# Kernel tuning notes

Hardware: AMD Instinct MI355X
Metric: run time of the kernel (lower is better)

The kernel has to match this reference:

```python
import jax, jax.numpy as jnp
import numpy as np

K = 2  # k-MIS hops (matches init k)


def _khop_min(mr, row, col, n, k):
    # k rounds of: min over in-neighbors (scatter_min row->col), then min with self
    for _ in range(k):
        neigh = jax.ops.segment_min(mr[row], col, num_segments=n)
        mr = jnp.minimum(mr, neigh)
    return mr


def _score_and_rank(x, lin_w, lin_b, row, col, n, k):
    score = jax.nn.sigmoid(x @ lin_w + lin_b)  # [n,1] linear scorer
    s = score[:, 0]
    # 'greedy' heuristic: s' = s / ((A+I)^k 1)
    ks = jnp.ones_like(s)
    for _ in range(k):
        ks = ks + jax.ops.segment_sum(ks[row], col, num_segments=n)
    upd = s / ks
    perm = jnp.argsort(-upd)  # descending: higher score -> lower rank
    rank = jnp.zeros(n, jnp.int32).at[perm].set(jnp.arange(n, dtype=jnp.int32))
    return score, rank


def _kmis_cluster(row, col, rank, n, k):
    nI = jnp.int32(n)

    def cond(state):
        return ~jnp.all(state[1])

    def body(state):
        mis, mask, mr = state
        mr = _khop_min(mr, row, col, n, k)
        mis = mis | (rank == mr)
        m = mis.astype(jnp.int32)
        for _ in range(k):  # propagate coverage k hops (scatter_max)
            neigh = jax.ops.segment_max(m[row], col, num_segments=n)
            m = jnp.maximum(m, jnp.clip(neigh, 0, 1))
        mask = m > 0
        mr = jnp.where(mask, nI, rank)
        return mis, mask, mr

    mis0 = jnp.zeros(n, bool)
    mis, _, _ = jax.lax.while_loop(cond, body, (mis0, mis0, rank))
    # clustering: propagate min rank of MIS nodes k hops
    mr = _khop_min(jnp.where(mis, rank, nI), row, col, n, k)
    mis_idx = jnp.nonzero(mis)[0]  # eager (data-dependent size, like torch)
    rank_mis = rank[mis_idx]
    order = jnp.argsort(rank_mis)
    # unique(min_rank).inverse then perm[clusters] == index into MIS nodes (node order)
    cluster = order[jnp.searchsorted(rank_mis[order], mr)]
    return mis_idx, cluster


def setup_inputs() -> dict:
    key = jax.random.key(0)
    k1, k2, k3, _ = jax.random.split(key, 4)
    n, e, d = 100000, 1600000, 256
    x = jax.random.normal(k1, (n, d), jnp.float32)
    edge_index = jax.random.randint(k2, (2, e), 0, n, jnp.int32)
    lin_w = jax.random.normal(k3, (d, 1), jnp.float32) * 0.05
    lin_b = jnp.zeros((1,), jnp.float32)
    return {"x": x, "edge_index": edge_index, "lin_w": lin_w, "lin_b": lin_b}


def reference(x, edge_index, lin_w, lin_b):
    n = x.shape[0]
    row, col = edge_index[0], edge_index[1]
    score, rank = _score_and_rank(x, lin_w, lin_b, row, col, n, K)
    mis_idx, cluster = _kmis_cluster(row, col, rank, n, K)
    # pool edges: relabel endpoints, coalesce duplicates with 'sum', drop self-loops
    pairs = jnp.stack([cluster[row], cluster[col]], axis=1)
    uniq, inv = jnp.unique(pairs, axis=0, return_inverse=True)
    val = jax.ops.segment_sum(jnp.ones(row.shape[0], jnp.float32), inv.reshape(-1), num_segments=uniq.shape[0])
    keep = uniq[:, 0] != uniq[:, 1]
    new_edge_index = uniq[keep].T
    new_edge_attr = val[keep]
    # pool nodes: score_passthrough='before', aggr_x=None -> select MIS rows
    x_pool = (x * score)[mis_idx]
    return x_pool, new_edge_index, new_edge_attr
```

## Files before the change

kernel.cpp:

```cpp
#include <hip/hip_runtime.h>
#include <math.h>

#define BLOCK 256
#define EGRID 2048
#define SG    512
#define NTHE (EGRID*BLOCK)
#define NWVE (NTHE/64)
#define INF_ 0x7fffffff
#define TB   6000
#define AWMAX 224
#define DENSE_ITERS 6

struct KParams {
  const float* x;
  const int*   ei;
  const float* w;
  const float* bb;
  float* out;
  int n, e, d, out_size;
  int* ws;
  long long ws_ints;
};

struct Lay {
  float* score; int *ks1,*cursor;
  int *keyA,*idxA,*keyB,*idxB,*lrank;
  int *rank,*mr,*t1,*mis,*mm,*misPre,*r2c,*clus,*colPtr,*rowPtr;
  unsigned *bh,*dtot,*dbase,*btot,*bbase;
  int *cnts,*colSrc,*rowDst,*pairCnt;
  long long unionBase;
};

__device__ __host__ inline Lay mklay(int* ws, int n, int e) {
  Lay L;
  L.score=(float*)ws;
  L.ks1   = ws + (size_t)1*n;
  L.cursor= ws + (size_t)2*n;
  L.keyA  = ws + (size_t)3*n;
  L.idxA  = ws + (size_t)4*n;
  L.keyB  = ws + (size_t)5*n;
  L.idxB  = ws + (size_t)6*n;
  L.lrank = ws + (size_t)7*n;
  L.rank  = ws + (size_t)8*n;
  L.mr    = ws + (size_t)9*n;
  L.t1    = ws + (size_t)10*n;
  L.mis   = ws + (size_t)11*n;
  L.mm    = ws + (size_t)12*n;
  L.misPre= ws + (size_t)13*n;
  L.r2c   = ws + (size_t)14*n;
  L.clus  = ws + (size_t)15*n;
  L.colPtr= ws + (size_t)16*n;
  L.rowPtr= ws + (size_t)17*n + 64;
  int* sm = ws + (size_t)18*n + 128;
  L.bh    = (unsigned*)sm;
  L.dtot  = L.bh + 256*SG;
  L.dbase = L.dtot + 256;
  L.btot  = L.dbase + 256;
  L.bbase = L.btot + SG;
  L.cnts  = (int*)(L.bbase + SG);
  L.unionBase = 18ll*n + 128 + 256ll*SG + 512 + 2ll*SG + 16;
  L.colSrc  = ws + L.unionBase;
  L.rowDst  = L.colSrc + e;
  L.pairCnt = ws + L.unionBase;
  return L;
}

__device__ inline int gmin_(const int* __restrict__ s, const int* __restrict__ val,
                            int p, int pe, int m) {
  for (; p+3 < pe; p += 4) {
    int a0=s[p],a1=s[p+1],a2=s[p+2],a3=s[p+3];
    int t0=val[a0],t1=val[a1],t2=val[a2],t3=val[a3];
    t0=min(t0,t1); t2=min(t2,t3); t0=min(t0,t2); if (t0<m) m=t0;
  }
  for (; p<pe; ++p){ int t=val[s[p]]; if (t<m) m=t; }
  return m;
}
__device__ inline int gor_(const int* __restrict__ s, const int* __restrict__ val,
                           int p, int pe, int m) {
  for (; p+3 < pe; p += 4) m |= val[s[p]] | val[s[p+1]] | val[s[p+2]] | val[s[p+3]];
  for (; p<pe; ++p) m |= val[s[p]];
  return m;
}
__device__ inline int gsum_(const int* __restrict__ s, const int* __restrict__ val,
                            int p, int pe, int m) {
  for (; p+3 < pe; p += 4) m += val[s[p]] + val[s[p+1]] + val[s[p+2]] + val[s[p+3]];
  for (; p<pe; ++p) m += val[s[p]];
  return m;
}

__device__ inline int btotPrefix(const unsigned* btot, int upto) {
  __shared__ int red[256];
  int tid = threadIdx.x;
  int partial = 0;
  for (int idx = tid; idx < upto; idx += 256) partial += (int)btot[idx];
  __syncthreads();
  red[tid] = partial; __syncthreads();
  for (int off = 128; off > 0; off >>= 1) { if (tid < off) red[tid] += red[tid+off]; __syncthreads(); }
  int r = red[0]; __syncthreads();
  return r;
}

__global__ __launch_bounds__(BLOCK) void k_score(KParams P) {
  Lay L = mklay(P.ws, P.n, P.e);
  int gid = blockIdx.x*BLOCK + threadIdx.x;
  int lane = gid & 63, gwv = gid >> 6;
  int d4 = P.d >> 2;
  double bconst = (double)P.bb[0];
  const float4* w4 = (const float4*)P.w;
  for (int v = gwv; v < P.n; v += NWVE) {
    const float4* xr = (const float4*)(P.x + (size_t)v*P.d);
    double s = 0.0;
    for (int q = lane; q < d4; q += 64) {
      float4 xv = xr[q], wv = w4[q];
      s += (double)xv.x*wv.x + (double)xv.y*wv.y + (double)xv.z*wv.z + (double)xv.w*wv.w;
    }
    for (int off = 32; off > 0; off >>= 1) s += __shfl_down(s, off);
    if (lane == 0) L.score[v] = (float)(1.0/(1.0+exp(-(s+bconst))));
  }
  for (int v = gid; v < P.n; v += NTHE) L.ks1[v] = 0;
}

__global__ __launch_bounds__(BLOCK) void k_degree(KParams P) {
  Lay L = mklay(P.ws, P.n, P.e);
  const int* col = P.ei + P.e;
  int gid = blockIdx.x*BLOCK + threadIdx.x;
  for (int j = gid; j < P.e; j += NTHE) atomicAdd(&L.ks1[col[j]], 1);
}

__global__ __launch_bounds__(BLOCK) void k_scan1(KParams P) {
  Lay L = mklay(P.ws, P.n, P.e);
  __shared__ int lds[256];
  int tid = threadIdx.x, bid = blockIdx.x;
  int chunk = (P.n + SG - 1)/SG;
  int ig = bid*chunk + tid;
  bool valid = (tid < chunk) && (ig < P.n);
  int v2 = valid ? L.ks1[ig] : 0;
  lds[tid] = v2; __syncthreads();
  for (int off = 1; off < 256; off <<= 1) {
    int t = (tid >= off) ? lds[tid-off] : 0; __syncthreads();
    lds[tid] += t; __syncthreads();
  }
  if (valid) L.colPtr[ig] = lds[tid] - v2;
  if (tid == 0) L.btot[bid] = (unsigned)lds[255];
}

__global__ __launch_bounds__(BLOCK) void k_scan3(KParams P) {
  Lay L = mklay(P.ws, P.n, P.e);
  int tid = threadIdx.x, bid = blockIdx.x;
  int base = btotPrefix(L.btot, bid);
  int chunk = (P.n + SG - 1)/SG;
  int ig = bid*chunk + tid;
  if (tid < chunk && ig < P.n) {
    int cp = L.colPtr[ig] + base;
    L.colPtr[ig] = cp; L.cursor[ig] = cp; L.ks1[ig] += 1;
  }
  if (bid == 0 && tid == 0) L.colPtr[P.n] = P.e;
}

__global__ __launch_bounds__(BLOCK) void k_csr(KParams P) {
  Lay L = mklay(P.ws, P.n, P.e);
  const int* row = P.ei; const int* col = P.ei + P.e;
  int gid = blockIdx.x*BLOCK + threadIdx.x;
  for (int j = gid; j < P.e; j += NTHE) {
    int pos = atomicAdd(&L.cursor[col[j]], 1);
    L.colSrc[pos] = row[j];
  }
}

__global__ __launch_bounds__(BLOCK) void k_keygen(KParams P) {
  Lay L = mklay(P.ws, P.n, P.e);
  int v = blockIdx.x*BLOCK + threadIdx.x;
  if (v >= P.n) return;
  int s = gsum_(L.colSrc, L.ks1, L.colPtr[v], L.colPtr[v+1], L.ks1[v]);
  float upd = L.score[v] / (float)s;
  unsigned u = __float_as_uint(upd);
  u = (u & 0x80000000u) ? (~u) : (u | 0x80000000u);
  ((unsigned*)L.keyA)[v] = ~u;
  ((unsigned*)L.idxA)[v] = (unsigned)v;
}

__global__ __launch_bounds__(BLOCK) void k_sort_local(KParams P, int pass) {
  Lay L = mklay(P.ws, P.n, P.e);
  __shared__ int ldsH[1024];
  int tid = threadIdx.x, bid = blockIdx.x, lane = tid & 63, wib = tid >> 6;
  unsigned* sk = (pass & 1) ? (unsigned*)L.keyB : (unsigned*)L.keyA;
  int shift = pass*8;
  for (int i = tid; i < 1024; i += BLOCK) ldsH[i] = 0;
  __syncthreads();
  int chunk = (P.n + SG - 1)/SG;
  int ig = bid*chunk + tid;
  bool valid = (tid < chunk) && (ig < P.n);
  int dig = 0;
  if (valid) dig = (int)((sk[ig] >> shift) & 255u);
  unsigned long long mmask = __ballot(valid);
  for (int b = 0; b < 8; ++b) {
    unsigned long long bm = __ballot((dig >> b) & 1);
    mmask &= ((dig >> b) & 1) ? bm : ~bm;
  }
  int lp = 0;
  if (valid) {
    lp = __popcll(mmask & ((1ull << lane) - 1ull));
    if (lp == 0) ldsH[wib*256 + dig] = __popcll(mmask);
  }
  __syncthreads();
  if (tid < 256) {
    int c0=ldsH[tid], c1=ldsH[256+tid], c2=ldsH[512+tid], c3=ldsH[768+tid];
    ldsH[tid]=0; ldsH[256+tid]=c0; ldsH[512+tid]=c0+c1; ldsH[768+tid]=c0+c1+c2;
    L.bh[(size_t)tid*SG + bid] = (unsigned)(c0+c1+c2+c3);
  }
  __syncthreads();
  if (valid) ((unsigned*)L.lrank)[ig] = (unsigned)(ldsH[wib*256 + dig] + lp);
}

__global__ __launch_bounds__(BLOCK) void k_sort_scan1(KParams P) {
  Lay L = mklay(P.ws, P.n, P.e);
  int g = blockIdx.x*BLOCK + threadIdx.x;
  int dg = g >> 6, lane = g & 63;
  if (dg >= 256) return;
  unsigned running = 0;
  for (int r = 0; r < SG/64; ++r) {
    unsigned v = L.bh[(size_t)dg*SG + r*64 + lane];
    unsigned incl = v;
    for (int off = 1; off < 64; off <<= 1) { unsigned t = __shfl_up(incl, off); if (lane >= off) incl += t; }
    L.bh[(size_t)dg*SG + r*64 + lane] = incl - v + running;
    running += __shfl(incl, 63);
  }
  if (lane == 0) L.dtot[dg] = running;
}

__global__ __launch_bounds__(BLOCK) void k_sort_scatter(KParams P, int pass) {
  Lay L = mklay(P.ws, P.n, P.e);
  __shared__ unsigned sdb[256];
  unsigned *sk,*si,*dk,*di;
  if (pass & 1) { sk=(unsigned*)L.keyB; si=(unsigned*)L.idxB; dk=(unsigned*)L.keyA; di=(unsigned*)L.idxA; }
  else          { sk=(unsigned*)L.keyA; si=(unsigned*)L.idxA; dk=(unsigned*)L.keyB; di=(unsigned*)L.idxB; }
  int tid = threadIdx.x, bid = blockIdx.x;
  unsigned myv = L.dtot[tid];
  sdb[tid] = myv; __syncthreads();
  for (int off = 1; off < 256; off <<= 1) {
    unsigned t = (tid >= off) ? sdb[tid-off] : 0u; __syncthreads();
    sdb[tid] += t; __syncthreads();
  }
  unsigned excl = sdb[tid] - myv; __syncthreads();
  sdb[tid] = excl; __syncthreads();
  int chunk = (P.n + SG - 1)/SG;
  int ig = bid*chunk + tid;
  if (tid < chunk && ig < P.n) {
    unsigned key = sk[ig];
    int dig = (int)((key >> (pass*8)) & 255u);
    unsigned pos = sdb[dig] + L.bh[(size_t)dig*SG + bid] + ((unsigned*)L.lrank)[ig];
    dk[pos] = key; di[pos] = si[ig];
  }
}

__global__ __launch_bounds__(BLOCK) void k_rankinit(KParams P) {
  Lay L = mklay(P.ws, P.n, P.e);
  int i = blockIdx.x*BLOCK + threadIdx.x;
  if (blockIdx.x == 0 && threadIdx.x == 0) {
    L.cnts[4] = P.n;
    L.cnts[5] = 0;
  }
  if (i >= P.n) return;
  int v = (int)((unsigned*)L.idxA)[i];
  L.rank[v] = i;
  L.mm[v] = i;
  L.mis[v] = 0;
}

__global__ __launch_bounds__(BLOCK) void k_dmin(KParams P, int t) {
  Lay L = mklay(P.ws, P.n, P.e);
  if (L.cnts[4+(t&1)] <= TB) return;
  int w = blockIdx.x*BLOCK + threadIdx.x;
  if (w >= P.n) return;
  L.mr[w] = gmin_(L.colSrc, L.mm, L.colPtr[w], L.colPtr[w+1], L.mm[w]);
}
__global__ __launch_bounds__(BLOCK) void k_dsel(KParams P, int t) {
  Lay L = mklay(P.ws, P.n, P.e);
  int q = t & 1;
  int A = L.cnts[4+q];
  if (A <= TB) return;
  int i = blockIdx.x*BLOCK + threadIdx.x;
  if (i >= A) return;
  int v = (t == 0) ? i : (q ? L.keyB : L.keyA)[i];
  int m2 = gmin_(L.colSrc, L.mr, L.colPtr[v], L.colPtr[v+1], L.mr[v]);
  if (L.rank[v] == m2) L.mis[v] = 1;
}
__global__ __launch_bounds__(BLOCK) void k_dor(KParams P, int t) {
  Lay L = mklay(P.ws, P.n, P.e);
  int q = t & 1;
  if (L.cnts[4+q] <= TB) return;
  int w = blockIdx.x*BLOCK + threadIdx.x;
  if (blockIdx.x == 0 && threadIdx.x == 0) L.cnts[4+(1-q)] = 0;
  if (w >= P.n) return;
  L.t1[w] = gor_(L.colSrc, L.mis, L.colPtr[w], L.colPtr[w+1], L.mis[w]);
}
__global__ __launch_bounds__(BLOCK) void k_drb(KParams P, int t) {
  Lay L = mklay(P.ws, P.n, P.e);
  int q = t & 1;
  int A = L.cnts[4+q];
  int* act  = (t == 0) ? (int*)0 : (q ? L.keyB : L.keyA);
  int* nact = q ? L.keyA : L.keyB;
  int gid = blockIdx.x*BLOCK + threadIdx.x;
  if (A <= TB) {
    for (int i = gid; i < A; i += (P.n + BLOCK - 1)/BLOCK*BLOCK) nact[i] = act[i];
    if (gid == 0) L.cnts[4+(1-q)] = A;
    return;
  }
  int lane = threadIdx.x & 63;
  bool aliveF = false; int v = 0;
  if (gid < A) {
    v = (t == 0) ? gid : act[gid];
    int dead = gor_(L.colSrc, L.t1, L.colPtr[v], L.colPtr[v+1], L.t1[v]);
    if (dead) L.mm[v] = INF_; else aliveF = true;
  }
  unsigned long long mk = __ballot(aliveF);
  int cntw = __popcll(mk);
  if (cntw) {
    int fl = __ffsll((unsigned long long)mk) - 1;
    int base = 0;
    if (lane == fl) base = atomicAdd(&L.cnts[4+(1-q)], cntw);
    base = __shfl(base, fl);
    if (aliveF) nact[base + __popcll(mk & ((1ull<<lane)-1ull))] = v;
  }
}

__global__ __launch_bounds__(BLOCK) void k_tcomp1(KParams P) {
  Lay L = mklay(P.ws, P.n, P.e);
  __shared__ int lds[256];
  int tid = threadIdx.x, bid = blockIdx.x;
  int chunk = (P.n + SG - 1)/SG;
  int ig = bid*chunk + tid;
  bool valid = (tid < chunk) && (ig < P.n);
  int f = 0;
  if (valid) { int v = (int)((unsigned*)L.idxA)[ig]; f = (L.mm[v] != INF_) ? 1 : 0; }
  lds[tid] = f; __syncthreads();
  for (int off = 1; off < 256; off <<= 1) {
    int t = (tid >= off) ? lds[tid-off] : 0; __syncthreads();
    lds[tid] += t; __syncthreads();
  }
  if (valid) L.t1[ig] = lds[tid] - f;
  if (tid == 0) L.btot[bid] = (unsigned)lds[255];
}
__global__ __launch_bounds__(BLOCK) void k_tcomp3(KParams P) {
  Lay L = mklay(P.ws, P.n, P.e);
  int tid = threadIdx.x, bid = blockIdx.x;
  int base = btotPrefix(L.btot, bid);
  int chunk = (P.n + SG - 1)/SG;
  int ig = bid*chunk + tid;
  if (tid < chunk && ig < P.n) {
    int v = (int)((unsigned*)L.idxA)[ig];
    if (L.mm[v] != INF_) {
      int pos = L.t1[ig] + base;
      L.lrank[pos] = v;
      L.cursor[v] = pos;
    } else L.cursor[v] = -1;
  }
  int A = L.cnts[4];
  if (A > 0) {
    int AW = (A + 31) >> 5;
    int AWP = (AW + 3) & ~3;
    unsigned* bs = (unsigned*)L.rowDst;
    long long tot = (long long)A * AWP;
    for (long long idx = (long long)bid*BLOCK + tid; idx < tot; idx += (long long)SG*BLOCK) bs[idx] = 0u;
  }
}
__global__ __launch_bounds__(BLOCK) void k_tbuild(KParams P) {
  Lay L = mklay(P.ws, P.n, P.e);
  int A = L.cnts[4];
  if (A <= 0) return;
  int AW = (A + 31) >> 5;
  int AWP = (AW + 3) & ~3;
  unsigned* bs = (unsigned*)L.rowDst;
  const int* __restrict__ cp = L.colPtr;
  const int* __restrict__ cs = L.colSrc;
  const int* __restrict__ nodeIdx = L.cursor;
  int gid = blockIdx.x*BLOCK + threadIdx.x;
  int lane = gid & 63, gwv = gid >> 6;
  int nW = (gridDim.x*BLOCK) >> 6;
  for (int i = gwv; i < A; i += nW) {
    int v = L.lrank[i];
    unsigned* row = bs + (size_t)i*AWP;
    if (lane == 0) atomicOr(&row[i >> 5], 1u << (i & 31));
    int p0 = cp[v], p1 = cp[v+1];
    for (int p = p0 + lane; p < p1; p += 64) {
      int u = cs[p];
      int j = nodeIdx[u];
      if (j >= 0) atomicOr(&row[j >> 5], 1u << (j & 31));
      int p3 = cp[u+1];
      for (int p2 = cp[u]; p2 < p3; ++p2) {
        int w2 = cs[p2];
        int j2 = nodeIdx[w2];
        if (j2 >= 0) atomicOr(&row[j2 >> 5], 1u << (j2 & 31));
      }
    }
  }
}
__global__ __launch_bounds__(1024) void k_trounds(KParams P) {
  Lay L = mklay(P.ws, P.n, P.e);
  __shared__ __align__(16) unsigned aliveW[AWMAX];
  __shared__ __align__(16) unsigned selW[AWMAX];
  __shared__ int scnt;
  int A = L.cnts[4];
  if (A <= 0) return;
  int AW = (A + 31) >> 5;
  int AWP = (AW + 3) & ~3;
  const unsigned* __restrict__ bs = (const unsigned*)L.rowDst;
  const int* __restrict__ S = L.lrank;
  const uint4* __restrict__ a4 = (const uint4*)aliveW;
  const uint4* __restrict__ s4 = (const uint4*)selW;
  int tid = threadIdx.x;
  for (int w = tid; w < AWP; w += 1024) {
    int base = w*32; int c = A - base;
    aliveW[w] = (c >= 32) ? 0xffffffffu : ((c > 0) ? ((1u << c) - 1u) : 0u);
  }
  __syncthreads();
  int ng = AWP >> 2;
  for (int rounds = 0; rounds < 8192; ++rounds) {
    for (int w = tid; w < AWP; w += 1024) selW[w] = 0u;
    if (tid == 0) scnt = 0;
    __syncthreads();
    for (int i = tid; i < A; i += 1024) {
      if ((aliveW[i>>5] >> (i&31)) & 1u) {
        const unsigned* __restrict__ row = bs + (size_t)i*AWP;
        const uint4* __restrict__ r4 = (const uint4*)row;
        int wl = i >> 5;
        int nf = wl >> 2;
        unsigned any = 0;
        int g = 0;
        for (; g + 2 <= nf; g += 2) {
          uint4 a = r4[g],   b = r4[g+1];
          uint4 av = a4[g],  bv = a4[g+1];
          unsigned r0 = (a.x&av.x)|(a.y&av.y)|(a.z&av.z)|(a.w&av.w);
          unsigned r1 = (b.x&bv.x)|(b.y&bv.y)|(b.z&bv.z)|(b.w&bv.w);
          any = r0 | r1;
          if (any) break;
        }
        if (!any && g < nf) {
          uint4 a = r4[g]; uint4 av = a4[g];
          any = (a.x&av.x)|(a.y&av.y)|(a.z&av.z)|(a.w&av.w);
        }
        if (!any) {
          for (int w2 = nf << 2; w2 < wl; ++w2) any |= row[w2] & aliveW[w2];
          if (!any && (i & 31)) any = row[wl] & aliveW[wl] & ((1u << (i&31)) - 1u);
        }
        if (!any) { atomicOr(&selW[i>>5], 1u << (i&31)); L.mis[S[i]] = 1; }
      }
    }
    __syncthreads();
    int surv = 0;
    for (int i = tid; i < A; i += 1024) {
      if ((aliveW[i>>5] >> (i&31)) & 1u) {
        const uint4* __restrict__ r4 = (const uint4*)(bs + (size_t)i*AWP);
        unsigned dead = 0;
        int g = 0;
        for (; g + 2 <= ng; g += 2) {
          uint4 a = r4[g],  b = r4[g+1];
          uint4 sa = s4[g], sb = s4[g+1];
          dead |= (a.x&sa.x)|(a.y&sa.y)|(a.z&sa.z)|(a.w&sa.w)
                | (b.x&sb.x)|(b.y&sb.y)|(b.z&sb.z)|(b.w&sb.w);
        }
        if (g < ng) {
          uint4 a = r4[g]; uint4 sa = s4[g];
          dead |= (a.x&sa.x)|(a.y&sa.y)|(a.z&sa.z)|(a.w&sa.w);
        }
        if (dead) atomicAnd(&aliveW[i>>5], ~(1u << (i&31)));
        else ++surv;
      }
    }
    if (surv) atomicAdd(&scnt, surv);
    __syncthreads();
    int sc = scnt;
    __syncthreads();
    if (sc == 0) break;
  }
}

__global__ __launch_bounds__(BLOCK) void k_scanM1(KParams P) {
  Lay L = mklay(P.ws, P.n, P.e);
  __shared__ int lds[256];
  int tid = threadIdx.x, bid = blockIdx.x;
  int chunk = (P.n + SG - 1)/SG;
  int ig = bid*chunk + tid;
  bool valid = (tid < chunk) && (ig < P.n);
  int v2 = 0;
  if (valid) {
    v2 = L.mis[ig];
    L.mm[ig] = v2 ? L.rank[ig] : P.n;
  }
  lds[tid] = v2; __syncthreads();
  for (int off = 1; off < 256; off <<= 1) {
    int t = (tid >= off) ? lds[tid-off] : 0; __syncthreads();
    lds[tid] += t; __syncthreads();
  }
  if (valid) L.misPre[ig] = lds[tid] - v2;
  if (tid == 0) L.btot[bid] = (unsigned)lds[255];
}
__global__ __launch_bounds__(BLOCK) void k_fin1(KParams P) {
  Lay L = mklay(P.ws, P.n, P.e);
  int v = blockIdx.x*BLOCK + threadIdx.x;
  if (v >= P.n) return;
  L.t1[v] = gmin_(L.colSrc, L.mm, L.colPtr[v], L.colPtr[v+1], L.mm[v]);
}
__global__ __launch_bounds__(BLOCK) void k_fin2(KParams P) {
  Lay L = mklay(P.ws, P.n, P.e);
  int v = blockIdx.x*BLOCK + threadIdx.x;
  if (v >= P.n) return;
  L.mr[v] = gmin_(L.colSrc, L.t1, L.colPtr[v], L.colPtr[v+1], L.t1[v]);
}
__global__ __launch_bounds__(BLOCK) void k_scanM3(KParams P) {
  Lay L = mklay(P.ws, P.n, P.e);
  int tid = threadIdx.x, bid = blockIdx.x;
  int base = btotPrefix(L.btot, bid);
  int total = btotPrefix(L.btot, SG);
  int chunk = (P.n + SG - 1)/SG;
  int ig = bid*chunk + tid;
  if (tid < chunk && ig < P.n) {
    int p = L.misPre[ig] + base;
    L.misPre[ig] = p;
    if (L.mis[ig]) L.r2c[L.rank[ig]] = p;
  }
  if (bid == 0 && tid == 0) L.cnts[2] = total;
}

__global__ __launch_bounds__(BLOCK) void k_clus(KParams P) {
  Lay L = mklay(P.ws, P.n, P.e);
  int gid = blockIdx.x*BLOCK + threadIdx.x;
  int M = L.cnts[2];
  long long M2 = (long long)M*M;
  for (int v = gid; v < P.n; v += NTHE) {
    int r3 = L.mr[v];
    L.clus[v] = (r3 >= 0 && r3 < P.n) ? L.r2c[r3] : 0;
  }
  bool pairOk = (M > 0) && (M2 < 0x7fffffffll) && (L.unionBase + M2 <= P.ws_ints);
  if (pairOk) {
    int m2i = (int)M2;
    for (int i = gid; i < m2i; i += NTHE) L.pairCnt[i] = 0;
  }
}

__global__ __launch_bounds__(BLOCK) void k_pair(KParams P) {
  Lay L = mklay(P.ws, P.n, P.e);
  int M = L.cnts[2];
  long long M2 = (long long)M*M;
  bool pairOk = (M > 0) && (M2 < 0x7fffffffll) && (L.unionBase + M2 <= P.ws_ints);
  if (!pairOk) return;
  const int* row = P.ei; const int* col = P.ei + P.e;
  int gid = blockIdx.x*BLOCK + threadIdx.x;
  for (int j = gid; j < P.e; j += NTHE) {
    int a = L.clus[row[j]], b2 = L.clus[col[j]];
    atomicAdd(&L.pairCnt[a*M + b2], 1);
  }
}

__global__ __launch_bounds__(BLOCK) void k_keep1(KParams P) {
  Lay L = mklay(P.ws, P.n, P.e);
  __shared__ int lds[256];
  int tid = threadIdx.x, bid = blockIdx.x;
  int M = L.cnts[2];
  long long M2 = (long long)M*M;
  bool pairOk = (M > 0) && (M2 < 0x7fffffffll) && (L.unionBase + M2 <= P.ws_ints);
  int m2i = pairOk ? (int)M2 : 0;
  int chunkP = pairOk ? (m2i + SG - 1)/SG : 0;
  int pstart = bid*chunkP; if (pstart > m2i) pstart = m2i;
  int pend = pstart + chunkP; if (pend > m2i) pend = m2i;
  int localKeep = 0;
  for (int i = pstart + tid; i < pend; i += BLOCK) {
    int c = L.pairCnt[i];
    if (c > 0 && (i / M) != (i % M)) ++localKeep;
  }
  lds[tid] = localKeep; __syncthreads();
  for (int off = 128; off > 0; off >>= 1) { if (tid < off) lds[tid] += lds[tid+off]; __syncthreads(); }
  if (tid == 0) L.btot[bid] = (unsigned)lds[0];
}

__global__ __launch_bounds__(BLOCK) void k_edges(KParams P) {
  Lay L = mklay(P.ws, P.n, P.e);
  __shared__ int lds[256];
  int tid = threadIdx.x, bid = blockIdx.x;
  int M = L.cnts[2];
  long long M2 = (long long)M*M;
  bool pairOk = (M > 0) && (M2 < 0x7fffffffll) && (L.unionBase + M2 <= P.ws_ints);
  if (!pairOk) return;
  int base = btotPrefix(L.btot, bid);
  int EK = btotPrefix(L.btot, SG);
  int m2i = (int)M2;
  int chunkP = (m2i + SG - 1)/SG;
  int pstart = bid*chunkP; if (pstart > m2i) pstart = m2i;
  int pend = pstart + chunkP; if (pend > m2i) pend = m2i;
  size_t eBase = (size_t)M * (size_t)P.d;
  bool outOk = (eBase + 3ull*(size_t)EK <= (size_t)P.out_size);
  int running2 = base;
  for (int t0 = pstart; t0 < pend; t0 += BLOCK) {
    int i = t0 + tid;
    int c = 0, kept = 0, a = 0, b2 = 0;
    if (i < pend) {
      c = L.pairCnt[i];
      a = i / M; b2 = i % M;
      kept = (c > 0 && a != b2) ? 1 : 0;
    }
    lds[tid] = kept; __syncthreads();
    for (int off = 1; off < 256; off <<= 1) {
      int t = (tid >= off) ? lds[tid-off] : 0; __syncthreads();
      lds[tid] += t; __syncthreads();
    }
    int incl = lds[tid], tot = lds[255];
    if (kept && outOk) {
      int j2 = running2 + incl - 1;
      P.out[eBase + (size_t)j2] = (float)a;
      P.out[eBase + (size_t)EK + (size_t)j2] = (float)b2;
      P.out[eBase + 2ull*(size_t)EK + (size_t)j2] = (float)c;
    }
    running2 += tot;
    __syncthreads();
  }
}

__global__ __launch_bounds__(BLOCK) void k_xpool(KParams P) {
  Lay L = mklay(P.ws, P.n, P.e);
  int gid = blockIdx.x*BLOCK + threadIdx.x;
  int lane = gid & 63, gwv = gid >> 6;
  int M = L.cnts[2];
  int d4 = P.d >> 2;
  size_t eBase = (size_t)M * (size_t)P.d;
  if (eBase > (size_t)P.out_size) return;
  for (int v = gwv; v < P.n; v += NWVE) {
    if (L.mis[v]) {
      int p = L.misPre[v];
      float sc = L.score[v];
      const float4* xr = (const float4*)(P.x + (size_t)v*P.d);
      float4* outr = (float4*)P.out + (size_t)p*d4;
      for (int q = lane; q < d4; q += 64) {
        float4 xv = xr[q];
        outr[q] = make_float4(xv.x*sc, xv.y*sc, xv.z*sc, xv.w*sc);
      }
    }
  }
}

extern "C" void kernel_launch(void* const* d_in, const int* in_sizes, int n_in,
                              void* d_out, int out_size, void* d_ws, size_t ws_size,
                              hipStream_t stream) {
  KParams P;
  P.x  = (const float*)d_in[0];
  P.ei = (const int*)d_in[1];
  P.w  = (const float*)d_in[2];
  P.bb = (const float*)d_in[3];
  P.out = (float*)d_out;
  P.d = in_sizes[2];
  P.n = in_sizes[0] / P.d;
  P.e = in_sizes[1] / 2;
  P.out_size = out_size;
  P.ws = (int*)d_ws;
  P.ws_ints = (long long)(ws_size / 4);
  const int nblk = (P.n + BLOCK - 1) / BLOCK;

  k_score <<<EGRID, BLOCK, 0, stream>>>(P);
  k_degree<<<EGRID, BLOCK, 0, stream>>>(P);
  k_scan1 <<<SG,    BLOCK, 0, stream>>>(P);
  k_scan3 <<<SG,    BLOCK, 0, stream>>>(P);
  k_csr   <<<EGRID, BLOCK, 0, stream>>>(P);
  k_keygen<<<nblk,  BLOCK, 0, stream>>>(P);
  for (int pass = 0; pass < 4; ++pass) {
    k_sort_local  <<<SG, BLOCK, 0, stream>>>(P, pass);
    k_sort_scan1  <<<64, BLOCK, 0, stream>>>(P);
    k_sort_scatter<<<SG, BLOCK, 0, stream>>>(P, pass);
  }
  k_rankinit<<<nblk, BLOCK, 0, stream>>>(P);
  for (int t = 0; t < DENSE_ITERS; ++t) {
    k_dmin <<<nblk, BLOCK, 0, stream>>>(P, t);
    k_dsel <<<nblk, BLOCK, 0, stream>>>(P, t);
    k_dor  <<<nblk, BLOCK, 0, stream>>>(P, t);
    k_drb  <<<nblk, BLOCK, 0, stream>>>(P, t);
  }
  k_tcomp1 <<<SG,   BLOCK, 0, stream>>>(P);
  k_tcomp3 <<<SG,   BLOCK, 0, stream>>>(P);
  k_tbuild <<<nblk, BLOCK, 0, stream>>>(P);
  k_trounds<<<1,    1024,  0, stream>>>(P);
  k_scanM1<<<SG, BLOCK, 0, stream>>>(P);
  k_fin1  <<<nblk, BLOCK, 0, stream>>>(P);
  k_fin2  <<<nblk, BLOCK, 0, stream>>>(P);
  k_scanM3<<<SG, BLOCK, 0, stream>>>(P);
  k_clus <<<EGRID, BLOCK, 0, stream>>>(P);
  k_pair <<<EGRID, BLOCK, 0, stream>>>(P);
  k_keep1<<<SG,    BLOCK, 0, stream>>>(P);
  k_edges<<<SG,    BLOCK, 0, stream>>>(P);
  k_xpool<<<EGRID, BLOCK, 0, stream>>>(P);
}
```

Before: 968.9 us.

## Build transposed conflict bitmatrix and kill nodes via selected-row OR in tail rounds

During the dense tail MIS phase, the build kernel now also fills a transposed bit matrix, when workspace allows, by issuing mirrored atomicOr operations. Each round records the selected nodes in a shared list. Dead nodes are then found by OR-ing the transposed rows of only those nodes into a shared deadW mask, instead of every alive node scanning its full row against the selection mask. A per-node resume pointer (pw) also lets the lower-rank check skip words already known to be clear. In exchange, the build does twice the atomics and writes a second matrix, the check loop drops its uint4 vectorization, and the resume pointer is stored as an unsigned char.

Measured after the change: 1.023 ms. 5.5% more time.

```diff
diff --git a/kernel.cpp b/kernel.cpp
--- a/kernel.cpp
+++ b/kernel.cpp
@@ -9,6 +9,7 @@
 #define INF_ 0x7fffffff
 #define TB   6000
 #define AWMAX 224
+#define TBCAP 7168
 #define DENSE_ITERS 6
 
 struct KParams {
@@ -362,6 +363,11 @@
     unsigned* bs = (unsigned*)L.rowDst;
     long long tot = (long long)A * AWP;
     for (long long idx = (long long)bid*BLOCK + tid; idx < tot; idx += (long long)SG*BLOCK) bs[idx] = 0u;
+    bool transOk = (L.unionBase + 2ll*P.e + tot <= P.ws_ints);
+    if (transOk) {
+      unsigned* tr = (unsigned*)(P.ws + L.unionBase + 2ll*P.e);
+      for (long long idx = (long long)bid*BLOCK + tid; idx < tot; idx += (long long)SG*BLOCK) tr[idx] = 0u;
+    }
   }
 }
 __global__ __launch_bounds__(BLOCK) void k_tbuild(KParams P) {
@@ -371,6 +377,8 @@
   int AW = (A + 31) >> 5;
   int AWP = (AW + 3) & ~3;
   unsigned* bs = (unsigned*)L.rowDst;
+  bool transOk = (L.unionBase + 2ll*P.e + (long long)A*AWP <= P.ws_ints);
+  unsigned* tr = transOk ? (unsigned*)(P.ws + L.unionBase + 2ll*P.e) : (unsigned*)0;
   const int* __restrict__ cp = L.colPtr;
   const int* __restrict__ cs = L.colSrc;
   const int* __restrict__ nodeIdx = L.cursor;
@@ -380,17 +388,28 @@
   for (int i = gwv; i < A; i += nW) {
     int v = L.lrank[i];
     unsigned* row = bs + (size_t)i*AWP;
-    if (lane == 0) atomicOr(&row[i >> 5], 1u << (i & 31));
+    unsigned ibit = 1u << (i & 31);
+    int iw = i >> 5;
+    if (lane == 0) {
+      atomicOr(&row[iw], ibit);
+      if (tr) atomicOr(&tr[(size_t)i*AWP + iw], ibit);
+    }
     int p0 = cp[v], p1 = cp[v+1];
     for (int p = p0 + lane; p < p1; p += 64) {
       int u = cs[p];
       int j = nodeIdx[u];
-      if (j >= 0) atomicOr(&row[j >> 5], 1u << (j & 31));
+      if (j >= 0) {
+        atomicOr(&row[j >> 5], 1u << (j & 31));
+        if (tr) atomicOr(&tr[(size_t)j*AWP + iw], ibit);
+      }
       int p3 = cp[u+1];
       for (int p2 = cp[u]; p2 < p3; ++p2) {
         int w2 = cs[p2];
         int j2 = nodeIdx[w2];
-        if (j2 >= 0) atomicOr(&row[j2 >> 5], 1u << (j2 & 31));
+        if (j2 >= 0) {
+          atomicOr(&row[j2 >> 5], 1u << (j2 & 31));
+          if (tr) atomicOr(&tr[(size_t)j2*AWP + iw], ibit);
+        }
       }
     }
   }
@@ -399,72 +418,81 @@
   Lay L = mklay(P.ws, P.n, P.e);
   __shared__ __align__(16) unsigned aliveW[AWMAX];
   __shared__ __align__(16) unsigned selW[AWMAX];
-  __shared__ int scnt;
+  __shared__ __align__(16) unsigned deadW[AWMAX];
+  __shared__ int selList[TBCAP];
+  __shared__ unsigned char pw[TBCAP];
+  __shared__ int scnt, selCnt;
   int A = L.cnts[4];
   if (A <= 0) return;
   int AW = (A + 31) >> 5;
   int AWP = (AW + 3) & ~3;
   const unsigned* __restrict__ bs = (const unsigned*)L.rowDst;
+  bool transOk = (L.unionBase + 2ll*P.e + (long long)A*AWP <= P.ws_ints);
+  const unsigned* __restrict__ tr = (const unsigned*)(P.ws + L.unionBase + 2ll*P.e);
   const int* __restrict__ S = L.lrank;
-  const uint4* __restrict__ a4 = (const uint4*)aliveW;
-  const uint4* __restrict__ s4 = (const uint4*)selW;
   int tid = threadIdx.x;
   for (int w = tid; w < AWP; w += 1024) {
     int base = w*32; int c = A - base;
     aliveW[w] = (c >= 32) ? 0xffffffffu : ((c > 0) ? ((1u << c) - 1u) : 0u);
   }
+  for (int i = tid; i < A; i += 1024) pw[i] = 0;
   __syncthreads();
-  int ng = AWP >> 2;
   for (int rounds = 0; rounds < 8192; ++rounds) {
-    for (int w = tid; w < AWP; w += 1024) selW[w] = 0u;
-    if (tid == 0) scnt = 0;
+    for (int w = tid; w < AWP; w += 1024) { selW[w] = 0u; deadW[w] = 0u; }
+    if (tid == 0) { scnt = 0; selCnt = 0; }
     __syncthreads();
     for (int i = tid; i < A; i += 1024) {
       if ((aliveW[i>>5] >> (i&31)) & 1u) {
         const unsigned* __restrict__ row = bs + (size_t)i*AWP;
-        const uint4* __restrict__ r4 = (const uint4*)row;
         int wl = i >> 5;
-        int nf = wl >> 2;
+        int g = pw[i];
         unsigned any = 0;
-        int g = 0;
-        for (; g + 2 <= nf; g += 2) {
-          uint4 a = r4[g],   b = r4[g+1];
-          uint4 av = a4[g],  bv = a4[g+1];
-          unsigned r0 = (a.x&av.x)|(a.y&av.y)|(a.z&av.z)|(a.w&av.w);
-          unsigned r1 = (b.x&bv.x)|(b.y&bv.y)|(b.z&bv.z)|(b.w&bv.w);
-          any = r0 | r1;
+        while (g < wl) {
+          any = row[g] & aliveW[g];
           if (any) break;
+          ++g;
         }
-        if (!any && g < nf) {
-          uint4 a = r4[g]; uint4 av = a4[g];
-          any = (a.x&av.x)|(a.y&av.y)|(a.z&av.z)|(a.w&av.w);
+        pw[i] = (unsigned char)g;
+        if (!any && (i & 31)) any = row[wl] & aliveW[wl] & ((1u << (i&31)) - 1u);
+        if (!any) {
+          int sp = atomicAdd(&selCnt, 1);
+          selList[sp] = i;
+          atomicOr(&selW[i>>5], 1u << (i&31));
+          L.mis[S[i]] = 1;
         }
-        if (!any) {
-          for (int w2 = nf << 2; w2 < wl; ++w2) any |= row[w2] & aliveW[w2];
-          if (!any && (i & 31)) any = row[wl] & aliveW[wl] & ((1u << (i&31)) - 1u);
+      }
+    }
+    __syncthreads();
+    int nsel = selCnt;
+    if (nsel == 0) break;
+    int surv = 0;
+    if (transOk) {
+      int w = tid & 255, qs = tid >> 8;
+      if (w < AW) {
+        unsigned acc = 0;
+        for (int q = qs; q < nsel; q += 4) acc |= tr[(size_t)selList[q]*AWP + w];
+        if (acc) atomicOr(&deadW[w], acc);
+      }
+      __syncthreads();
+      for (int w2 = tid; w2 < AW; w2 += 1024) {
+        unsigned na = aliveW[w2] & ~deadW[w2];
+        aliveW[w2] = na;
+        surv += __popc(na);
+      }
+    } else {
+      for (int i = tid; i < A; i += 1024) {
+        if ((aliveW[i>>5] >> (i&31)) & 1u) {
+          const uint4* __restrict__ r4 = (const uint4*)(bs + (size_t)i*AWP);
+          const uint4* __restrict__ s4 = (const uint4*)selW;
+          unsigned dead = 0;
+          int ng = AWP >> 2;
+          for (int g2 = 0; g2 < ng; ++g2) {
+            uint4 a = r4[g2], sa = s4[g2];
+            dead |= (a.x&sa.x)|(a.y&sa.y)|(a.z&sa.z)|(a.w&sa.w);
+          }
+          if (dead) atomicAnd(&aliveW[i>>5], ~(1u << (i&31)));
+          else ++surv;
         }
-        if (!any) { atomicOr(&selW[i>>5], 1u << (i&31)); L.mis[S[i]] = 1; }
-      }
-    }
-    __syncthreads();
-    int surv = 0;
-    for (int i = tid; i < A; i += 1024) {
-      if ((aliveW[i>>5] >> (i&31)) & 1u) {
-        const uint4* __restrict__ r4 = (const uint4*)(bs + (size_t)i*AWP);
-        unsigned dead = 0;
-        int g = 0;
-        for (; g + 2 <= ng; g += 2) {
-          uint4 a = r4[g],  b = r4[g+1];
-          uint4 sa = s4[g], sb = s4[g+1];
-          dead |= (a.x&sa.x)|(a.y&sa.y)|(a.z&sa.z)|(a.w&sa.w)
-                | (b.x&sb.x)|(b.y&sb.y)|(b.z&sb.z)|(b.w&sb.w);
-        }
-        if (g < ng) {
-          uint4 a = r4[g]; uint4 sa = s4[g];
-          dead |= (a.x&sa.x)|(a.y&sa.y)|(a.z&sa.z)|(a.w&sa.w);
-        }
-        if (dead) atomicAnd(&aliveW[i>>5], ~(1u << (i&31)));
-        else ++surv;
       }
     }
     if (surv) atomicAdd(&scnt, surv);
```
